# Performance work log

Measured on AMD Instinct MI355X. Metric: run time of the kernel, lower is better.

Reference implementation:

```python
import jax, jax.numpy as jnp
import numpy as np

# Reconstructed from DAT's DAttentionBaseline with the wrapper's config:
# q_size=(14,14), n_heads=12, n_head_channels=64, n_groups=8, stride=1,
# offset_range_factor=1.0, use_pe=False (so log_cpb/rpe unused), no_off=False,
# ksize=3, dropout=0 (eval). Followed by the wrapper's Linear out-projection.

H = W = 14
G = 8          # n_groups
NH = 12        # n_heads
OFF_RANGE_FACTOR = 1.0


def grid_sample_bilinear(img, grid):
    # img: [B, C, H, W]; grid: [B, Hg, Wg, 2] in (x, y) order, [-1, 1],
    # align_corners=True, padding_mode='zeros' (torch defaults used by DAT).
    B, C, Hi, Wi = img.shape
    gx = (grid[..., 0] + 1.0) * 0.5 * (Wi - 1)
    gy = (grid[..., 1] + 1.0) * 0.5 * (Hi - 1)
    x0 = jnp.floor(gx)
    y0 = jnp.floor(gy)
    x1 = x0 + 1.0
    y1 = y0 + 1.0
    wx1 = gx - x0
    wx0 = 1.0 - wx1
    wy1 = gy - y0
    wy0 = 1.0 - wy1
    flat = img.reshape(B, C, Hi * Wi)

    def tap(xi, yi, wgt):
        valid = (xi >= 0) & (xi <= Wi - 1) & (yi >= 0) & (yi <= Hi - 1)
        xi_c = jnp.clip(xi, 0, Wi - 1).astype(jnp.int32)
        yi_c = jnp.clip(yi, 0, Hi - 1).astype(jnp.int32)
        idx = (yi_c * Wi + xi_c).reshape(B, 1, -1)
        vals = jnp.take_along_axis(flat, idx, axis=2)  # [B, C, Hg*Wg]
        w = (wgt * valid.astype(img.dtype)).reshape(B, 1, -1)
        return vals * w

    out = (tap(x0, y0, wx0 * wy0) + tap(x1, y0, wx1 * wy0)
           + tap(x0, y1, wx0 * wy1) + tap(x1, y1, wx1 * wy1))
    return out  # [B, C, Hg*Wg]


def setup_inputs() -> dict:
    key = jax.random.key(0)
    ks = jax.random.split(key, 16)
    B, N, C = 128, 196, 768
    Cg = C // G  # 96
    s = 0.02
    return {
        "hidden_states": jax.random.normal(ks[0], (B, N, C), jnp.float32),
        "Wq": jax.random.normal(ks[1], (C, C), jnp.float32) * s,
        "bq": jnp.zeros((C,), jnp.float32),
        "off_dw_w": jax.random.normal(ks[2], (Cg, 1, 3, 3), jnp.float32) * s,
        "off_dw_b": jnp.zeros((Cg,), jnp.float32),
        "ln_w": jnp.ones((Cg,), jnp.float32),
        "ln_b": jnp.zeros((Cg,), jnp.float32),
        "off_pw_w": jax.random.normal(ks[3], (2, Cg), jnp.float32) * s,
        "Wk": jax.random.normal(ks[4], (C, C), jnp.float32) * s,
        "bk": jnp.zeros((C,), jnp.float32),
        "Wv": jax.random.normal(ks[5], (C, C), jnp.float32) * s,
        "bv": jnp.zeros((C,), jnp.float32),
        "Wproj": jax.random.normal(ks[6], (C, C), jnp.float32) * s,
        "bproj": jnp.zeros((C,), jnp.float32),
        "Wout": jax.random.normal(ks[7], (C, C), jnp.float32) * s,
        "bout": jnp.zeros((C,), jnp.float32),
    }


def reference(hidden_states, Wq, bq, off_dw_w, off_dw_b, ln_w, ln_b, off_pw_w,
              Wk, bk, Wv, bv, Wproj, bproj, Wout, bout):
    B, N, C = hidden_states.shape
    Cg = C // G
    nh, dh = NH, C // NH
    scale = dh ** -0.5
    dt = hidden_states.dtype

    x_im = hidden_states.reshape(B, H, W, C).transpose(0, 3, 1, 2)  # [B,C,H,W]

    # proj_q: 1x1 conv
    q_im = jnp.einsum('bchw,oc->bohw', x_im, Wq) + bq[None, :, None, None]
    q_off = q_im.reshape(B * G, Cg, H, W)

    # offset net: depthwise 3x3 conv -> LayerNorm(channels) -> GELU -> 1x1 (no bias)
    t = jax.lax.conv_general_dilated(
        q_off, off_dw_w, (1, 1), [(1, 1), (1, 1)],
        dimension_numbers=('NCHW', 'OIHW', 'NCHW'), feature_group_count=Cg)
    t = t + off_dw_b[None, :, None, None]
    mu = t.mean(axis=1, keepdims=True)
    var = ((t - mu) ** 2).mean(axis=1, keepdims=True)
    t = (t - mu) * jax.lax.rsqrt(var + 1e-5)
    t = t * ln_w[None, :, None, None] + ln_b[None, :, None, None]
    t = jax.nn.gelu(t, approximate=False)
    off = jnp.einsum('bchw,oc->bohw', t, off_pw_w)  # [B*G, 2(y,x), H, W]

    off_range = jnp.array([1.0 / (H - 1), 1.0 / (W - 1)], dt).reshape(1, 2, 1, 1)
    off = jnp.tanh(off) * off_range * OFF_RANGE_FACTOR
    off = off.transpose(0, 2, 3, 1)  # [B*G, H, W, 2] (y, x)

    ry = ((jnp.arange(H, dtype=dt) + 0.5) / H) * 2.0 - 1.0
    rx = ((jnp.arange(W, dtype=dt) + 0.5) / W) * 2.0 - 1.0
    ref = jnp.stack(jnp.meshgrid(ry, rx, indexing='ij'), axis=-1)  # [H,W,2]
    pos = off + ref[None]          # (y, x)
    grid = pos[..., ::-1]          # (x, y) for grid_sample

    x_g = x_im.reshape(B * G, Cg, H, W)
    n_sample = H * W
    x_s = grid_sample_bilinear(x_g, grid).reshape(B, C, n_sample)

    k = jnp.einsum('bcn,oc->bon', x_s, Wk) + bk[None, :, None]
    v = jnp.einsum('bcn,oc->bon', x_s, Wv) + bv[None, :, None]

    qh = q_im.reshape(B, nh, dh, N)
    kh = k.reshape(B, nh, dh, n_sample)
    vh = v.reshape(B, nh, dh, n_sample)

    attn = jax.nn.softmax(jnp.einsum('bhcm,bhcn->bhmn', qh, kh) * scale, axis=-1)
    out = jnp.einsum('bhmn,bhcn->bhcm', attn, vh).reshape(B, C, N)

    y = jnp.einsum('bcn,oc->bon', out, Wproj) + bproj[None, :, None]
    y = y.transpose(0, 2, 1)               # [B, N, C]
    y = y @ Wout.T + bout                  # wrapper's Linear out-projection
    return y, attn
```

## Files before the change

### kernel.cpp

```cpp
#include <hip/hip_runtime.h>
#include <math.h>

#define Bsz 128
#define Hh 14
#define Ww 14
#define Nn 196
#define Cc 768
#define Gg 8
#define CgC 96
#define NHh 12
#define Dh 64
#define ROWS (Bsz*Nn)

typedef _Float16 half8 __attribute__((ext_vector_type(8)));
typedef _Float16 half4 __attribute__((ext_vector_type(4)));
typedef float f32x4 __attribute__((ext_vector_type(4)));

__global__ __launch_bounds__(256) void cvt_f32_f16(
    const float* __restrict__ src, _Float16* __restrict__ dst, int n8)
{
  const int i = blockIdx.x * 256 + threadIdx.x;
  if (i >= n8) return;
  float4 a = *(const float4*)(src + (size_t)i * 8);
  float4 b = *(const float4*)(src + (size_t)i * 8 + 4);
  half8 h;
  h[0]=(_Float16)a.x; h[1]=(_Float16)a.y; h[2]=(_Float16)a.z; h[3]=(_Float16)a.w;
  h[4]=(_Float16)b.x; h[5]=(_Float16)b.y; h[6]=(_Float16)b.z; h[7]=(_Float16)b.w;
  *(half8*)(dst + (size_t)i * 8) = h;
}

__global__ __launch_bounds__(256) void cvt_w5(
    const float* __restrict__ w0, const float* __restrict__ w1,
    const float* __restrict__ w2, const float* __restrict__ w3,
    const float* __restrict__ w4, _Float16* __restrict__ dst)
{
  const int i = blockIdx.x * 256 + threadIdx.x;
  const int per = Cc * Cc / 8;
  if (i >= 5 * per) return;
  const int m = i / per, r = i - m * per;
  const float* s = (m == 0) ? w0 : (m == 1) ? w1 : (m == 2) ? w2 : (m == 3) ? w3 : w4;
  float4 a = *(const float4*)(s + (size_t)r * 8);
  float4 b = *(const float4*)(s + (size_t)r * 8 + 4);
  half8 h;
  h[0]=(_Float16)a.x; h[1]=(_Float16)a.y; h[2]=(_Float16)a.z; h[3]=(_Float16)a.w;
  h[4]=(_Float16)b.x; h[5]=(_Float16)b.y; h[6]=(_Float16)b.z; h[7]=(_Float16)b.w;
  *(half8*)(dst + (size_t)m * Cc * Cc + (size_t)r * 8) = h;
}

template<int F16OUT>
__global__ __launch_bounds__(256) void gemm_h16(
    const _Float16* __restrict__ A, const _Float16* __restrict__ W,
    const float* __restrict__ bias, void* __restrict__ Cout)
{
  __shared__ __align__(16) _Float16 As[128 * 64];
  __shared__ __align__(16) _Float16 Bs[128 * 64];
  const int t = threadIdx.x;
  const int nwg = gridDim.x;
  int bid = blockIdx.x;
  bid = (bid & 7) * (nwg >> 3) + (bid >> 3);
  const int colb = bid % 6, rowb = bid / 6;
  const int row0 = rowb * 128, col0 = colb * 128;
  const int lane = t & 63, w = t >> 6;
  const int wr = w >> 1, wc = w & 1;
  const int l15 = lane & 15, l4 = lane >> 4;
  const int srow = t >> 3;
  const int sg   = t & 7;

  f32x4 acc[4][4];
#pragma unroll
  for (int i = 0; i < 4; ++i)
#pragma unroll
    for (int j = 0; j < 4; ++j) acc[i][j] = (f32x4){0.f, 0.f, 0.f, 0.f};

  for (int kt = 0; kt < 12; ++kt) {
    const int k0 = kt * 64;
#pragma unroll
    for (int it = 0; it < 4; ++it) {
      const int r = it * 32 + srow;
      half8 ha = *(const half8*)(A + (size_t)(row0 + r) * Cc + k0 + sg * 8);
      half8 hw = *(const half8*)(W + (size_t)(col0 + r) * Cc + k0 + sg * 8);
      const int dst = r * 64 + ((sg ^ (r & 7)) * 8);
      *(half8*)&As[dst] = ha;
      *(half8*)&Bs[dst] = hw;
    }
    __syncthreads();
#pragma unroll
    for (int ks = 0; ks < 2; ++ks) {
      half8 af[4], bf[4];
#pragma unroll
      for (int mi = 0; mi < 4; ++mi) {
        const int r = wr * 64 + mi * 16 + l15;
        const int g = ks * 4 + l4;
        af[mi] = *(const half8*)&As[r * 64 + ((g ^ (r & 7)) * 8)];
      }
#pragma unroll
      for (int ni = 0; ni < 4; ++ni) {
        const int r = wc * 64 + ni * 16 + l15;
        const int g = ks * 4 + l4;
        bf[ni] = *(const half8*)&Bs[r * 64 + ((g ^ (r & 7)) * 8)];
      }
#pragma unroll
      for (int mi = 0; mi < 4; ++mi)
#pragma unroll
        for (int ni = 0; ni < 4; ++ni)
          acc[mi][ni] = __builtin_amdgcn_mfma_f32_16x16x32_f16(af[mi], bf[ni], acc[mi][ni], 0, 0, 0);
    }
    __syncthreads();
  }

#pragma unroll
  for (int ni = 0; ni < 4; ++ni) {
    const int col = col0 + wc * 64 + ni * 16 + l15;
    const float bcol = bias[col];
#pragma unroll
    for (int mi = 0; mi < 4; ++mi) {
      f32x4 v = acc[mi][ni];
      const int rbase = row0 + wr * 64 + mi * 16 + l4 * 4;
#pragma unroll
      for (int r = 0; r < 4; ++r) {
        if (F16OUT) {
          ((_Float16*)Cout)[(size_t)(rbase + r) * Cc + col] = (_Float16)(v[r] + bcol);
        } else {
          ((float*)Cout)[(size_t)(rbase + r) * Cc + col] = v[r] + bcol;
        }
      }
    }
  }
}

__global__ __launch_bounds__(512, 4) void offset_sample(
    const _Float16* __restrict__ Q16, const float* __restrict__ hidden,
    const float* __restrict__ dw_w, const float* __restrict__ dw_b,
    const float* __restrict__ ln_w, const float* __restrict__ ln_b,
    const float* __restrict__ pw_w, _Float16* __restrict__ XS)
{
  __shared__ float Qs[Nn * CgC];
  const int tid = threadIdx.x;
  const int g = blockIdx.x;
  const int b = blockIdx.y;
  const int cl = tid & 31;
  const int grp = tid >> 5;

  const size_t base = (size_t)b * Nn * Cc + g * CgC;
  for (int i = tid; i < Nn * 12; i += 512) {
    const int n = i / 12, j = i - n * 12;
    half8 hv = *(const half8*)(Q16 + base + (size_t)n * Cc + j * 8);
#pragma unroll
    for (int e = 0; e < 8; ++e) Qs[n * CgC + j * 8 + e] = (float)hv[e];
  }

  float wdw[3][9], bdw[3], wln[3], bln[3], wp0[3], wp1[3];
#pragma unroll
  for (int k = 0; k < 3; ++k) {
    const int c = cl + k * 32;
#pragma unroll
    for (int t9 = 0; t9 < 9; ++t9) wdw[k][t9] = dw_w[c * 9 + t9];
    bdw[k] = dw_b[c];
    wln[k] = ln_w[c];
    bln[k] = ln_b[c];
    wp0[k] = pw_w[c];
    wp1[k] = pw_w[CgC + c];
  }
  __syncthreads();

  const float* hb0 = hidden + base;

  for (int s0 = 0; s0 < Nn; s0 += 16) {
    const int site = s0 + grp;
    if (site >= Nn) break;
    const int h = site / Ww, w = site % Ww;

    float t[3];
#pragma unroll
    for (int k = 0; k < 3; ++k) t[k] = bdw[k];
#pragma unroll
    for (int ky = 0; ky < 3; ++ky) {
      const int hp = h + ky - 1;
      if (hp < 0 || hp > Hh - 1) continue;
#pragma unroll
      for (int kx = 0; kx < 3; ++kx) {
        const int wp = w + kx - 1;
        if (wp < 0 || wp > Ww - 1) continue;
        const float* row = &Qs[(hp * Ww + wp) * CgC + cl];
#pragma unroll
        for (int k = 0; k < 3; ++k)
          t[k] = fmaf(row[k * 32], wdw[k][ky * 3 + kx], t[k]);
      }
    }

    float s = t[0] + t[1] + t[2];
#pragma unroll
    for (int off = 1; off <= 16; off <<= 1) s += __shfl_xor(s, off, 32);
    const float mu = s * (1.f / 96.f);
    float d2 = 0.f;
#pragma unroll
    for (int k = 0; k < 3; ++k) { const float d = t[k] - mu; d2 = fmaf(d, d, d2); }
#pragma unroll
    for (int off = 1; off <= 16; off <<= 1) d2 += __shfl_xor(d2, off, 32);
    const float rstd = rsqrtf(d2 * (1.f / 96.f) + 1e-5f);

    float p0 = 0.f, p1 = 0.f;
#pragma unroll
    for (int k = 0; k < 3; ++k) {
      const float tn = (t[k] - mu) * rstd * wln[k] + bln[k];
      const float a = 0.5f * tn * (1.f + erff(tn * 0.70710678118654752f));
      p0 = fmaf(a, wp0[k], p0);
      p1 = fmaf(a, wp1[k], p1);
    }
#pragma unroll
    for (int off = 1; off <= 16; off <<= 1) {
      p0 += __shfl_xor(p0, off, 32);
      p1 += __shfl_xor(p1, off, 32);
    }

    const float offy = tanhf(p0) * (1.f / 13.f);
    const float offx = tanhf(p1) * (1.f / 13.f);
    const float refy = (h + 0.5f) / 14.f * 2.f - 1.f;
    const float refx = (w + 0.5f) / 14.f * 2.f - 1.f;
    const float gx = ((offx + refx) + 1.f) * 0.5f * 13.f;
    const float gy = ((offy + refy) + 1.f) * 0.5f * 13.f;

    const float x0f = floorf(gx), y0f = floorf(gy);
    const int x0 = (int)x0f, y0 = (int)y0f;
    const float wx1 = gx - x0f, wx0 = 1.f - wx1;
    const float wy1 = gy - y0f, wy0 = 1.f - wy1;
    const bool vx0 = (x0 >= 0) & (x0 <= 13), vx1 = (x0 + 1 >= 0) & (x0 + 1 <= 13);
    const bool vy0 = (y0 >= 0) & (y0 <= 13), vy1 = (y0 + 1 >= 0) & (y0 + 1 <= 13);
    float acc[3] = {0.f, 0.f, 0.f};
#pragma unroll
    for (int k = 0; k < 3; ++k) {
      const int c = cl + k * 32;
      if (vx0 & vy0) acc[k] = fmaf(wx0 * wy0, hb0[(size_t)(y0 * Ww + x0) * Cc + c], acc[k]);
      if (vx1 & vy0) acc[k] = fmaf(wx1 * wy0, hb0[(size_t)(y0 * Ww + x0 + 1) * Cc + c], acc[k]);
      if (vx0 & vy1) acc[k] = fmaf(wx0 * wy1, hb0[(size_t)((y0 + 1) * Ww + x0) * Cc + c], acc[k]);
      if (vx1 & vy1) acc[k] = fmaf(wx1 * wy1, hb0[(size_t)((y0 + 1) * Ww + x0 + 1) * Cc + c], acc[k]);
    }
    _Float16* xp = XS + ((size_t)b * Nn + site) * Cc + g * CgC + cl;
#pragma unroll
    for (int k = 0; k < 3; ++k) xp[k * 32] = (_Float16)acc[k];
  }
}

__global__ __launch_bounds__(512) void attn_fused(
    const _Float16* __restrict__ Qm, const _Float16* __restrict__ Km,
    const _Float16* __restrict__ Vm, float* __restrict__ attn,
    _Float16* __restrict__ OUT)
{
  __shared__ __align__(16) _Float16 Kt[208 * 72];
  __shared__ __align__(16) _Float16 Vt[64 * 232];
  __shared__ __align__(16) _Float16 Sl[8][16 * 232];
  const int tid = threadIdx.x;
  const int hh = blockIdx.x, b = blockIdx.y;
  const int lane = tid & 63, wv = tid >> 6;
  const int l15 = lane & 15, l4 = lane >> 4;

  const _Float16* Qbase = Qm + (size_t)b * Nn * Cc + hh * Dh;
  const _Float16* Kbase = Km + (size_t)b * Nn * Cc + hh * Dh;
  const _Float16* Vbase = Vm + (size_t)b * Nn * Cc + hh * Dh;

  {
    const int g = tid & 7;
    for (int n = tid >> 3; n < 208; n += 64) {
      half8 hv = {};
      if (n < Nn) hv = *(const half8*)(Kbase + (size_t)n * Cc + g * 8);
      *(half8*)&Kt[n * 72 + g * 8] = hv;
    }
  }
  {
    const int d0 = (tid & 15) * 4;
    for (int n = tid >> 4; n < Nn; n += 32) {
      half4 v = *(const half4*)(Vbase + (size_t)n * Cc + d0);
      Vt[(d0 + 0) * 232 + n] = v[0];
      Vt[(d0 + 1) * 232 + n] = v[1];
      Vt[(d0 + 2) * 232 + n] = v[2];
      Vt[(d0 + 3) * 232 + n] = v[3];
    }
    for (int e = tid; e < 64 * 36; e += 512) {
      int d = e / 36, n = Nn + e % 36;
      Vt[d * 232 + n] = (_Float16)0.f;
    }
  }
  for (int e = lane; e < 16 * 24; e += 64) {
    int m = e / 24, c = 208 + e % 24;
    Sl[wv][m * 232 + c] = (_Float16)0.f;
  }
  __syncthreads();

  for (int mt = wv; mt < 13; mt += 8) {
    const int qrow = mt * 16 + l15;
    const _Float16* qp = Qbase + (size_t)(qrow < Nn ? qrow : (Nn - 1)) * Cc + l4 * 8;
    half8 aq0 = *(const half8*)qp;
    half8 aq1 = *(const half8*)(qp + 32);

    f32x4 accs[13];
#pragma unroll
    for (int nt = 0; nt < 13; ++nt) accs[nt] = (f32x4){0.f, 0.f, 0.f, 0.f};
#pragma unroll
    for (int nt = 0; nt < 13; ++nt) {
      const int rb = (nt * 16 + l15) * 72;
      half8 bk0 = *(const half8*)&Kt[rb + l4 * 8];
      half8 bk1 = *(const half8*)&Kt[rb + 32 + l4 * 8];
      accs[nt] = __builtin_amdgcn_mfma_f32_16x16x32_f16(aq0, bk0, accs[nt], 0, 0, 0);
      accs[nt] = __builtin_amdgcn_mfma_f32_16x16x32_f16(aq1, bk1, accs[nt], 0, 0, 0);
    }

    float rmax[4] = {-1e30f, -1e30f, -1e30f, -1e30f};
#pragma unroll
    for (int nt = 0; nt < 13; ++nt) {
#pragma unroll
      for (int r = 0; r < 4; ++r) {
        float s = accs[nt][r] * 0.125f;
        if (nt == 12 && l15 >= 4) s = -1e30f;
        accs[nt][r] = s;
        rmax[r] = fmaxf(rmax[r], s);
      }
    }
#pragma unroll
    for (int off = 1; off <= 8; off <<= 1)
#pragma unroll
      for (int r = 0; r < 4; ++r)
        rmax[r] = fmaxf(rmax[r], __shfl_xor(rmax[r], off, 64));

    float rsum[4] = {0.f, 0.f, 0.f, 0.f};
#pragma unroll
    for (int nt = 0; nt < 13; ++nt) {
#pragma unroll
      for (int r = 0; r < 4; ++r) {
        float p = __expf(accs[nt][r] - rmax[r]);
        accs[nt][r] = p;
        rsum[r] += p;
      }
    }
#pragma unroll
    for (int off = 1; off <= 8; off <<= 1)
#pragma unroll
      for (int r = 0; r < 4; ++r)
        rsum[r] += __shfl_xor(rsum[r], off, 64);
    float rinv[4];
#pragma unroll
    for (int r = 0; r < 4; ++r) rinv[r] = 1.f / rsum[r];

    float* ab = attn + (((size_t)b * NHh + hh) * Nn) * (size_t)Nn;
#pragma unroll
    for (int nt = 0; nt < 13; ++nt) {
      const int n = nt * 16 + l15;
#pragma unroll
      for (int r = 0; r < 4; ++r) {
        float pr = accs[nt][r] * rinv[r];
        Sl[wv][(l4 * 4 + r) * 232 + n] = (_Float16)pr;
        const int m = mt * 16 + l4 * 4 + r;
        if (m < Nn && n < Nn) ab[(size_t)m * Nn + n] = pr;
      }
    }

    f32x4 acco[4];
#pragma unroll
    for (int dt = 0; dt < 4; ++dt) acco[dt] = (f32x4){0.f, 0.f, 0.f, 0.f};
#pragma unroll
    for (int nsl = 0; nsl < 7; ++nsl) {
      half8 ap = *(const half8*)&Sl[wv][l15 * 232 + nsl * 32 + l4 * 8];
#pragma unroll
      for (int dt = 0; dt < 4; ++dt) {
        half8 bv = *(const half8*)&Vt[(dt * 16 + l15) * 232 + nsl * 32 + l4 * 8];
        acco[dt] = __builtin_amdgcn_mfma_f32_16x16x32_f16(ap, bv, acco[dt], 0, 0, 0);
      }
    }
#pragma unroll
    for (int dt = 0; dt < 4; ++dt) {
#pragma unroll
      for (int r = 0; r < 4; ++r) {
        const int m = mt * 16 + l4 * 4 + r;
        if (m < Nn)
          OUT[((size_t)b * Nn + m) * Cc + hh * Dh + dt * 16 + l15] = (_Float16)acco[dt][r];
      }
    }
  }
}

extern "C" void kernel_launch(void* const* d_in, const int* in_sizes, int n_in,
                              void* d_out, int out_size, void* d_ws, size_t ws_size,
                              hipStream_t stream) {
  const float* hidden = (const float*)d_in[0];
  const float* Wq = (const float*)d_in[1];
  const float* bq = (const float*)d_in[2];
  const float* dw_w = (const float*)d_in[3];
  const float* dw_b = (const float*)d_in[4];
  const float* ln_w = (const float*)d_in[5];
  const float* ln_b = (const float*)d_in[6];
  const float* pw_w = (const float*)d_in[7];
  const float* Wk = (const float*)d_in[8];
  const float* bk = (const float*)d_in[9];
  const float* Wv = (const float*)d_in[10];
  const float* bv = (const float*)d_in[11];
  const float* Wp = (const float*)d_in[12];
  const float* bp = (const float*)d_in[13];
  const float* Wo = (const float*)d_in[14];
  const float* bo = (const float*)d_in[15];

  const size_t SZ = (size_t)Bsz * Nn * Cc;
  float* yout = (float*)d_out;
  float* attn = yout + SZ;

  _Float16* h16   = (_Float16*)d_ws;
  _Float16* Q16   = h16   + SZ;
  _Float16* XS16  = Q16   + SZ;
  _Float16* K16   = XS16  + SZ;
  _Float16* V16   = K16   + SZ;
  _Float16* OUT16 = V16   + SZ;
  _Float16* Y116  = OUT16 + SZ;
  _Float16* W16   = Y116  + SZ;

  const int gemm_blocks = (ROWS / 128) * (Cc / 128);
  const int n8 = (int)(SZ / 8);

  cvt_f32_f16<<<(n8 + 255) / 256, 256, 0, stream>>>(hidden, h16, n8);
  cvt_w5<<<(5 * Cc * Cc / 8 + 255) / 256, 256, 0, stream>>>(Wq, Wk, Wv, Wp, Wo, W16);

  gemm_h16<1><<<gemm_blocks, 256, 0, stream>>>(h16, W16 + 0 * (size_t)Cc * Cc, bq, Q16);
  offset_sample<<<dim3(Gg, Bsz), 512, 0, stream>>>(Q16, hidden, dw_w, dw_b, ln_w, ln_b, pw_w, XS16);
  gemm_h16<1><<<gemm_blocks, 256, 0, stream>>>(XS16, W16 + 1 * (size_t)Cc * Cc, bk, K16);
  gemm_h16<1><<<gemm_blocks, 256, 0, stream>>>(XS16, W16 + 2 * (size_t)Cc * Cc, bv, V16);
  attn_fused<<<dim3(NHh, Bsz), 512, 0, stream>>>(Q16, K16, V16, attn, OUT16);
  gemm_h16<1><<<gemm_blocks, 256, 0, stream>>>(OUT16, W16 + 3 * (size_t)Cc * Cc, bp, Y116);
  gemm_h16<0><<<gemm_blocks, 256, 0, stream>>>(Y116, W16 + 4 * (size_t)Cc * Cc, bo, yout);
}
```

Before: 569.2 us.

## Fuse K and V projections into one GEMM and shrink attention P staging

Replaces the two separate K and V projection GEMMs with one kernel that treats the concatenated Wk|Wv weights as a 1536-wide output and routes each column block to K16 or V16. This saves a launch and lets the sampled XS tile be reused across both projections within one grid. In the attention kernel, the per-wave 16x232 probability buffer becomes a 16x40 slice that is refilled per 32-column step from registers, and launch bounds of 4 blocks are requested. The smaller LDS footprint is meant to raise occupancy, at the cost of more small LDS writes and register pressure from keeping the probabilities in registers.

Measured after the change: 544.9 us. 1.04x faster.

```diff
diff --git a/kernel.cpp b/kernel.cpp
--- a/kernel.cpp
+++ b/kernel.cpp
@@ -128,6 +128,86 @@
   }
 }
 
+__global__ __launch_bounds__(256) void gemm_h16_kv(
+    const _Float16* __restrict__ A, const _Float16* __restrict__ Wkv,
+    const float* __restrict__ bk, const float* __restrict__ bv,
+    _Float16* __restrict__ K16, _Float16* __restrict__ V16)
+{
+  __shared__ __align__(16) _Float16 As[128 * 64];
+  __shared__ __align__(16) _Float16 Bs[128 * 64];
+  const int t = threadIdx.x;
+  const int nwg = gridDim.x;
+  int bid = blockIdx.x;
+  bid = (bid & 7) * (nwg >> 3) + (bid >> 3);
+  const int colb = bid % 12, rowb = bid / 12;
+  const int row0 = rowb * 128, col0 = colb * 128;
+  const int lane = t & 63, w = t >> 6;
+  const int wr = w >> 1, wc = w & 1;
+  const int l15 = lane & 15, l4 = lane >> 4;
+  const int srow = t >> 3;
+  const int sg   = t & 7;
+
+  _Float16* Cout = (colb < 6) ? K16 : V16;
+  const float* bias = (colb < 6) ? bk : bv;
+  const int cadj = (colb < 6) ? 0 : Cc;
+
+  f32x4 acc[4][4];
+#pragma unroll
+  for (int i = 0; i < 4; ++i)
+#pragma unroll
+    for (int j = 0; j < 4; ++j) acc[i][j] = (f32x4){0.f, 0.f, 0.f, 0.f};
+
+  for (int kt = 0; kt < 12; ++kt) {
+    const int k0 = kt * 64;
+#pragma unroll
+    for (int it = 0; it < 4; ++it) {
+      const int r = it * 32 + srow;
+      half8 ha = *(const half8*)(A + (size_t)(row0 + r) * Cc + k0 + sg * 8);
+      half8 hw = *(const half8*)(Wkv + (size_t)(col0 + r) * Cc + k0 + sg * 8);
+      const int dst = r * 64 + ((sg ^ (r & 7)) * 8);
+      *(half8*)&As[dst] = ha;
+      *(half8*)&Bs[dst] = hw;
+    }
+    __syncthreads();
+#pragma unroll
+    for (int ks = 0; ks < 2; ++ks) {
+      half8 af[4], bf[4];
+#pragma unroll
+      for (int mi = 0; mi < 4; ++mi) {
+        const int r = wr * 64 + mi * 16 + l15;
+        const int g = ks * 4 + l4;
+        af[mi] = *(const half8*)&As[r * 64 + ((g ^ (r & 7)) * 8)];
+      }
+#pragma unroll
+      for (int ni = 0; ni < 4; ++ni) {
+        const int r = wc * 64 + ni * 16 + l15;
+        const int g = ks * 4 + l4;
+        bf[ni] = *(const half8*)&Bs[r * 64 + ((g ^ (r & 7)) * 8)];
+      }
+#pragma unroll
+      for (int mi = 0; mi < 4; ++mi)
+#pragma unroll
+        for (int ni = 0; ni < 4; ++ni)
+          acc[mi][ni] = __builtin_amdgcn_mfma_f32_16x16x32_f16(af[mi], bf[ni], acc[mi][ni], 0, 0, 0);
+    }
+    __syncthreads();
+  }
+
+#pragma unroll
+  for (int ni = 0; ni < 4; ++ni) {
+    const int col = col0 + wc * 64 + ni * 16 + l15;
+    const float bcol = bias[col - cadj];
+#pragma unroll
+    for (int mi = 0; mi < 4; ++mi) {
+      f32x4 v = acc[mi][ni];
+      const int rbase = row0 + wr * 64 + mi * 16 + l4 * 4;
+#pragma unroll
+      for (int r = 0; r < 4; ++r)
+        Cout[(size_t)(rbase + r) * Cc + (col - cadj)] = (_Float16)(v[r] + bcol);
+    }
+  }
+}
+
 __global__ __launch_bounds__(512, 4) void offset_sample(
     const _Float16* __restrict__ Q16, const float* __restrict__ hidden,
     const float* __restrict__ dw_w, const float* __restrict__ dw_b,
@@ -241,14 +321,14 @@
   }
 }
 
-__global__ __launch_bounds__(512) void attn_fused(
+__global__ __launch_bounds__(512, 4) void attn_fused(
     const _Float16* __restrict__ Qm, const _Float16* __restrict__ Km,
     const _Float16* __restrict__ Vm, float* __restrict__ attn,
     _Float16* __restrict__ OUT)
 {
   __shared__ __align__(16) _Float16 Kt[208 * 72];
   __shared__ __align__(16) _Float16 Vt[64 * 232];
-  __shared__ __align__(16) _Float16 Sl[8][16 * 232];
+  __shared__ __align__(16) _Float16 Ps[8][16 * 40];
   const int tid = threadIdx.x;
   const int hh = blockIdx.x, b = blockIdx.y;
   const int lane = tid & 63, wv = tid >> 6;
@@ -280,10 +360,6 @@
       Vt[d * 232 + n] = (_Float16)0.f;
     }
   }
-  for (int e = lane; e < 16 * 24; e += 64) {
-    int m = e / 24, c = 208 + e % 24;
-    Sl[wv][m * 232 + c] = (_Float16)0.f;
-  }
   __syncthreads();
 
   for (int mt = wv; mt < 13; mt += 8) {
@@ -347,7 +423,7 @@
 #pragma unroll
       for (int r = 0; r < 4; ++r) {
         float pr = accs[nt][r] * rinv[r];
-        Sl[wv][(l4 * 4 + r) * 232 + n] = (_Float16)pr;
+        accs[nt][r] = pr;
         const int m = mt * 16 + l4 * 4 + r;
         if (m < Nn && n < Nn) ab[(size_t)m * Nn + n] = pr;
       }
@@ -358,7 +434,20 @@
     for (int dt = 0; dt < 4; ++dt) acco[dt] = (f32x4){0.f, 0.f, 0.f, 0.f};
 #pragma unroll
     for (int nsl = 0; nsl < 7; ++nsl) {
-      half8 ap = *(const half8*)&Sl[wv][l15 * 232 + nsl * 32 + l4 * 8];
+#pragma unroll
+      for (int h2 = 0; h2 < 2; ++h2) {
+        const int nt = nsl * 2 + h2;
+        if (nt < 13) {
+#pragma unroll
+          for (int r = 0; r < 4; ++r)
+            Ps[wv][(l4 * 4 + r) * 40 + h2 * 16 + l15] = (_Float16)accs[nt][r];
+        } else {
+#pragma unroll
+          for (int r = 0; r < 4; ++r)
+            Ps[wv][(l4 * 4 + r) * 40 + h2 * 16 + l15] = (_Float16)0.f;
+        }
+      }
+      half8 ap = *(const half8*)&Ps[wv][l15 * 40 + l4 * 8];
 #pragma unroll
       for (int dt = 0; dt < 4; ++dt) {
         half8 bv = *(const half8*)&Vt[(dt * 16 + l15) * 232 + nsl * 32 + l4 * 8];
@@ -411,6 +500,7 @@
   _Float16* W16   = Y116  + SZ;
 
   const int gemm_blocks = (ROWS / 128) * (Cc / 128);
+  const int kv_blocks   = (ROWS / 128) * 12;
   const int n8 = (int)(SZ / 8);
 
   cvt_f32_f16<<<(n8 + 255) / 256, 256, 0, stream>>>(hidden, h16, n8);
@@ -418,8 +508,7 @@
 
   gemm_h16<1><<<gemm_blocks, 256, 0, stream>>>(h16, W16 + 0 * (size_t)Cc * Cc, bq, Q16);
   offset_sample<<<dim3(Gg, Bsz), 512, 0, stream>>>(Q16, hidden, dw_w, dw_b, ln_w, ln_b, pw_w, XS16);
-  gemm_h16<1><<<gemm_blocks, 256, 0, stream>>>(XS16, W16 + 1 * (size_t)Cc * Cc, bk, K16);
-  gemm_h16<1><<<gemm_blocks, 256, 0, stream>>>(XS16, W16 + 2 * (size_t)Cc * Cc, bv, V16);
+  gemm_h16_kv<<<kv_blocks, 256, 0, stream>>>(XS16, W16 + 1 * (size_t)Cc * Cc, bk, bv, K16, V16);
   attn_fused<<<dim3(NHh, Bsz), 512, 0, stream>>>(Q16, K16, V16, attn, OUT16);
   gemm_h16<1><<<gemm_blocks, 256, 0, stream>>>(OUT16, W16 + 3 * (size_t)Cc * Cc, bp, Y116);
   gemm_h16<0><<<gemm_blocks, 256, 0, stream>>>(Y116, W16 + 4 * (size_t)Cc * Cc, bo, yout);
```
